# Performance work log

Measured on AMD Instinct MI355X. Metric: run time of the kernel, lower is better.

Reference implementation:

```python
import jax, jax.numpy as jnp
import numpy as np
from math import sqrt

N = 8192      # points
I = 16        # in_channels
H = 64        # hidden_units
O = 64        # out_channels
CUTS = 8      # conv MLP intermediate width
RADIUS = 9.0
GROUPS = 4    # GroupNorm groups
BLK = 128     # i-block size for tiled pairwise reduction (KeOps-style)


def _leaky(x):
    return jnp.where(x >= 0, x, 0.2 * x)


def _group_norm(f, w, b, eps=1e-5):
    # torch GroupNorm applied to (1, C, N): stats per group over (C//G channels x N points)
    n, c = f.shape
    g = f.reshape(n, GROUPS, c // GROUPS)
    m = g.mean(axis=(0, 2), keepdims=True)
    v = ((g - m) ** 2).mean(axis=(0, 2), keepdims=True)
    g = (g - m) * jax.lax.rsqrt(v + eps)
    return g.reshape(n, c) * w + b


def setup_inputs() -> dict:
    key = jax.random.key(0)
    ks = jax.random.split(key, 20)
    U = lambda k, s, lim: jax.random.uniform(k, s, minval=-lim, maxval=lim)
    points = jax.random.normal(ks[0], (N, 3), dtype=jnp.float32)
    nuv = jax.random.normal(ks[1], (N, 3, 3), dtype=jnp.float32)
    features = jax.random.normal(ks[2], (N, I), dtype=jnp.float32)
    # net_in (torch Linear default init)
    W_in1 = U(ks[3], (H, I), 1 / np.sqrt(I)); b_in1 = U(ks[4], (H,), 1 / np.sqrt(I))
    W_in2 = U(ks[5], (H, H), 1 / np.sqrt(H)); b_in2 = U(ks[6], (H,), 1 / np.sqrt(H))
    # conv MLP with custom init from the module
    A1 = jax.random.normal(ks[7], (CUTS, 3), dtype=jnp.float32)
    B1 = jax.random.uniform(ks[8], (CUTS,)) * 0.8 * jnp.sqrt((A1 ** 2).sum(-1))
    A2 = U(ks[9], (H, CUTS), 1 / np.sqrt(CUTS))
    B2 = jax.random.normal(ks[10], (H,)) * 0.5 * jnp.sqrt((A2 ** 2).sum(-1))
    # net_out
    W_out1 = U(ks[11], (O, H), 1 / np.sqrt(H)); b_out1 = U(ks[12], (O,), 1 / np.sqrt(H))
    W_out2 = U(ks[13], (O, O), 1 / np.sqrt(O)); b_out2 = U(ks[14], (O,), 1 / np.sqrt(O))
    return {
        "points": points, "nuv": nuv, "features": features,
        "W_in1": W_in1, "b_in1": b_in1, "W_in2": W_in2, "b_in2": b_in2,
        "gn_in_w": jnp.ones((H,), jnp.float32), "gn_in_b": jnp.zeros((H,), jnp.float32),
        "A1": A1, "B1": B1, "A2": A2, "B2": B2,
        "W_out1": W_out1, "b_out1": b_out1, "W_out2": W_out2, "b_out2": b_out2,
        "gn_out_w": jnp.ones((O,), jnp.float32), "gn_out_b": jnp.zeros((O,), jnp.float32),
    }


def _forward(points, nuv, features, W_in1, b_in1, W_in2, b_in2, gn_in_w, gn_in_b,
             A1, B1, A2, B2, W_out1, b_out1, W_out2, b_out2, gn_out_w, gn_out_b):
    # 1. net_in + GroupNorm
    f = _leaky(features @ W_in1.T + b_in1)
    f = _leaky(f @ W_in2.T + b_in2)
    f = _group_norm(f, gn_in_w, gn_in_b)          # (N, H)
    # 2. quasi-geodesic interaction, tiled over i-blocks (KeOps-style)
    pts = points / (sqrt(2.0) * RADIUS)
    normals = jax.lax.stop_gradient(nuv[:, 0, :])  # n_j is detached in the original
    nblk = N // BLK

    def body(carry, blk):
        xi, nuvi = blk                              # (B,3), (B,3,3)
        ni = nuvi[:, 0, :]                          # (B,3) n_i (not detached)
        diff = pts[None, :, :] - xi[:, None, :]     # (B,N,3) x_j - x_i
        dn = ni @ normals.T                         # (B,N) <n_i, n_j>
        d2 = (diff ** 2).sum(-1) * (2.0 - dn) ** 2  # pseudo-geodesic squared dist
        w = jnp.exp(-d2)                            # Gaussian window
        X = jnp.einsum('bij,bnj->bni', nuvi, diff)  # coords in local basis (B,N,3)
        h = jax.nn.relu(jnp.einsum('bnj,cj->bnc', X, A1) + B1)   # (B,N,CUTS)
        g = jax.nn.relu(jnp.einsum('bnc,hc->bnh', h, A2) + B2)   # (B,N,H)
        out = jnp.einsum('bn,bnh,nh->bh', w, g, f)  # sum_j w_ij * conv(P_ij) * f_j
        return carry, out

    _, outs = jax.lax.scan(
        body, None, (pts.reshape(nblk, BLK, 3), nuv.reshape(nblk, BLK, 3, 3)))
    f2 = outs.reshape(N, H)
    # 3. net_out + GroupNorm
    f2 = _leaky(f2 @ W_out1.T + b_out1)
    f2 = _leaky(f2 @ W_out2.T + b_out2)
    f2 = _group_norm(f2, gn_out_w, gn_out_b)       # (N, O)
    return f2


def reference(points, nuv, features, W_in1, b_in1, W_in2, b_in2, gn_in_w, gn_in_b,
              A1, B1, A2, B2, W_out1, b_out1, W_out2, b_out2, gn_out_w, gn_out_b):
    return _forward(points, nuv, features, W_in1, b_in1, W_in2, b_in2, gn_in_w, gn_in_b,
                    A1, B1, A2, B2, W_out1, b_out1, W_out2, b_out2, gn_out_w, gn_out_b)
```

## Files before the change

kernel.cpp:

```cpp
#include <hip/hip_runtime.h>
#include <hip/hip_bf16.h>
#include <stdint.h>


#define N_PTS   8192
#define CHUNK   64
#define NCHUNK  (N_PTS / CHUNK)
#define WPB     8
#define PSCALE  0.07856742013183861f
#define GN_CNT  (N_PTS * 16)

#define OFF_POINTS 0
#define OFF_NUV    24576
#define OFF_FEAT   98304
#define OFF_WIN1   229376
#define OFF_BIN1   230400
#define OFF_WIN2   230464
#define OFF_BIN2   234560
#define OFF_GNIW   234624
#define OFF_GNIB   234688
#define OFF_A1     234752
#define OFF_B1     234776
#define OFF_A2     234784
#define OFF_B2     235296
#define OFF_WOUT1  235360
#define OFF_BOUT1  239456
#define OFF_WOUT2  239520
#define OFF_BOUT2  243616
#define OFF_GNOW   243680
#define OFF_GNOB   243744
#define CVT_TOTAL  243808
#define NSEG 19

typedef _Float16 half2_t __attribute__((ext_vector_type(2)));
typedef _Float16 f16x8   __attribute__((ext_vector_type(8)));
typedef float    f32x2   __attribute__((ext_vector_type(2)));
typedef float    f32x4   __attribute__((ext_vector_type(4)));

struct InPtrs { const void* p[NSEG]; };

__device__ __forceinline__ float rfl(float x) {
  return __int_as_float(__builtin_amdgcn_readfirstlane(__float_as_int(x)));
}
__device__ __forceinline__ float leaky(float x) { return x > 0.f ? x : 0.2f * x; }

#if __has_builtin(__builtin_amdgcn_cvt_pkrtz)
__device__ __forceinline__ half2_t pk16(float a, float b) {
  return __builtin_bit_cast(half2_t, __builtin_amdgcn_cvt_pkrtz(a, b));
}
#else
__device__ __forceinline__ half2_t pk16(float a, float b) {
  half2_t r; r.x = (_Float16)a; r.y = (_Float16)b; return r;
}
#endif

__global__ __launch_bounds__(256) void prep_kernel(InPtrs ptrs, float* dst,
                                                   float* gstats) {
  if (blockIdx.x == 0 && threadIdx.x < 16) gstats[threadIdx.x] = 0.f;
  const uint32_t w0 = ((const uint32_t*)ptrs.p[7])[0];
  const bool bf = (w0 != 0x3F800000u);
  const int CUM[NSEG + 1] = {0, 24576, 98304, 229376, 230400, 230464, 234560,
                             234624, 234688, 234752, 234776, 234784, 235296,
                             235360, 239456, 239520, 243616, 243680, 243744,
                             243808};
  for (int e = blockIdx.x * 256 + threadIdx.x; e < CVT_TOTAL;
       e += gridDim.x * 256) {
    int s = 0;
#pragma unroll
    for (int i = 1; i < NSEG; ++i) s += (e >= CUM[i]) ? 1 : 0;
    const int rem = e - CUM[s];
    float v = bf ? __bfloat162float(((const __hip_bfloat16*)ptrs.p[s])[rem])
                 : ((const float*)ptrs.p[s])[rem];
    if (s == 0) v *= PSCALE;
    dst[e] = v;
  }
}

__global__ __launch_bounds__(256) void pack_kernel(
    const float* __restrict__ pool, float4* __restrict__ ppk,
    float4* __restrict__ npk) {
  const int n = blockIdx.x * 256 + threadIdx.x;
  const float px = pool[OFF_POINTS + n * 3 + 0];
  const float py = pool[OFF_POINTS + n * 3 + 1];
  const float pz = pool[OFF_POINTS + n * 3 + 2];
  float4 p; p.x = px; p.y = py; p.z = pz;
  p.w = fmaf(px, px, fmaf(py, py, pz * pz));
  ppk[n] = p;
  float4 q;
  q.x = pool[OFF_NUV + n * 9 + 0];
  q.y = pool[OFF_NUV + n * 9 + 1];
  q.z = pool[OFF_NUV + n * 9 + 2];
  q.w = 0.f;
  npk[n] = q;
}

__global__ __launch_bounds__(256) void mlp_in_kernel(
    const float* __restrict__ pool, float* __restrict__ fbuf) {
  __shared__ float ls[4][64];
  const int t = threadIdx.x, nl = t >> 6, h = t & 63;
  const int n = blockIdx.x * 4 + nl;
  const float4* fr = (const float4*)(pool + OFF_FEAT + n * 16);
  const float4* w1 = (const float4*)(pool + OFF_WIN1 + h * 16);
  float a = pool[OFF_BIN1 + h];
#pragma unroll
  for (int k = 0; k < 4; ++k) {
    const float4 x = fr[k], w = w1[k];
    a = fmaf(x.x, w.x, a); a = fmaf(x.y, w.y, a);
    a = fmaf(x.z, w.z, a); a = fmaf(x.w, w.w, a);
  }
  ls[nl][h] = leaky(a);
  __syncthreads();
  const float4* w2 = (const float4*)(pool + OFF_WIN2 + h * 64);
  const float4* lr = (const float4*)&ls[nl][0];
  float c = pool[OFF_BIN2 + h];
#pragma unroll
  for (int k = 0; k < 16; ++k) {
    const float4 x = lr[k], w = w2[k];
    c = fmaf(x.x, w.x, c); c = fmaf(x.y, w.y, c);
    c = fmaf(x.z, w.z, c); c = fmaf(x.w, w.w, c);
  }
  fbuf[n * 64 + h] = leaky(c);
}

__global__ __launch_bounds__(256) void mlp_out_kernel(
    const float* __restrict__ cbuf, const float* __restrict__ pool,
    float* __restrict__ obuf) {
  __shared__ float ls[4][64];
  const int t = threadIdx.x, nl = t >> 6, h = t & 63;
  const int n = blockIdx.x * 4 + nl;
  const float4* cr = (const float4*)(cbuf + n * 64);
  const float4* w1 = (const float4*)(pool + OFF_WOUT1 + h * 64);
  float a = pool[OFF_BOUT1 + h];
#pragma unroll
  for (int k = 0; k < 16; ++k) {
    const float4 x = cr[k], w = w1[k];
    a = fmaf(x.x, w.x, a); a = fmaf(x.y, w.y, a);
    a = fmaf(x.z, w.z, a); a = fmaf(x.w, w.w, a);
  }
  ls[nl][h] = leaky(a);
  __syncthreads();
  const float4* w2 = (const float4*)(pool + OFF_WOUT2 + h * 64);
  const float4* lr = (const float4*)&ls[nl][0];
  float c = pool[OFF_BOUT2 + h];
#pragma unroll
  for (int k = 0; k < 16; ++k) {
    const float4 x = lr[k], w = w2[k];
    c = fmaf(x.x, w.x, c); c = fmaf(x.y, w.y, c);
    c = fmaf(x.z, w.z, c); c = fmaf(x.w, w.w, c);
  }
  obuf[n * 64 + h] = leaky(c);
}

__global__ __launch_bounds__(256) void gn_stats_kernel(
    const float* __restrict__ buf, float* __restrict__ gstats) {
  __shared__ float red[8];
  const int t = threadIdx.x;
  const int g = (t & 63) >> 4;
  if (t < 8) red[t] = 0.f;
  float s = 0.f, q = 0.f;
  for (int idx = blockIdx.x * 256 + t; idx < N_PTS * 64; idx += 64 * 256) {
    const float v = buf[idx];
    s += v; q = fmaf(v, v, q);
  }
  __syncthreads();
  atomicAdd(&red[g], s);
  atomicAdd(&red[4 + g], q);
  __syncthreads();
  if (t < 8) atomicAdd(&gstats[t], red[t]);
}

__global__ __launch_bounds__(256) void gn_apply_Q_kernel(
    const float* __restrict__ buf, const float* __restrict__ gstats,
    const float* __restrict__ pool, float4* __restrict__ bufq) {
  __shared__ float tile[64][68];
  const int t = threadIdx.x;
  const int c = blockIdx.x;
  const int n0 = c * 64;
  const int rr = t >> 4;
  const int cc4 = (t & 15) * 4;
  const int g = cc4 >> 4;
  const float m = gstats[g] * (1.f / GN_CNT);
  const float v = gstats[4 + g] * (1.f / GN_CNT) - m * m;
  const float rs = rsqrtf(fmaxf(v, 0.f) + 1e-5f);
  const float4 gw = *(const float4*)&pool[OFF_GNIW + cc4];
  const float4 gb = *(const float4*)&pool[OFF_GNIB + cc4];
#pragma unroll
  for (int r = 0; r < 4; ++r) {
    const int row = rr + 16 * r;
    const float4 x = *(const float4*)&buf[(n0 + row) * 64 + cc4];
    float4 o;
    o.x = fmaf((x.x - m) * rs, gw.x, gb.x);
    o.y = fmaf((x.y - m) * rs, gw.y, gb.y);
    o.z = fmaf((x.z - m) * rs, gw.z, gb.z);
    o.w = fmaf((x.w - m) * rs, gw.w, gb.w);
    *(float4*)&tile[row][cc4] = o;
  }
  __syncthreads();
#pragma unroll
  for (int si = 0; si < 4; ++si) {
    const int s = t + 256 * si;
    const int region = s >> 6, lane = s & 63;
    const int jt = region >> 2, ht = region & 3;
    const int kg = lane >> 4, l15 = lane & 15;
    const int jb = 16 * jt + 4 * kg, h = 16 * ht + l15;
    float4 o;
    o.x = tile[jb + 0][h];
    o.y = tile[jb + 1][h];
    o.z = tile[jb + 2][h];
    o.w = tile[jb + 3][h];
    bufq[c * 1024 + s] = o;
  }
}

__global__ __launch_bounds__(256) void gn_apply_out_kernel(
    const float* __restrict__ buf, const float* __restrict__ gstats,
    const float* __restrict__ pool, void* __restrict__ out,
    const uint32_t* __restrict__ dref) {
  const bool bf = (dref[0] != 0x3F800000u);
  const int idx = blockIdx.x * 256 + threadIdx.x;
  const int h = idx & 63, g = h >> 4;
  const float m = gstats[g] * (1.f / GN_CNT);
  const float v = gstats[4 + g] * (1.f / GN_CNT) - m * m;
  const float rs = rsqrtf(fmaxf(v, 0.f) + 1e-5f);
  const float r = fmaf((buf[idx] - m) * rs, pool[OFF_GNOW + h], pool[OFF_GNOB + h]);
  if (bf) ((__hip_bfloat16*)out)[idx] = __float2bfloat16(r);
  else    ((float*)out)[idx] = r;
}

__global__ __launch_bounds__(512, 8) void conv_kernel(
    const float* __restrict__ pool, const float4* __restrict__ fq,
    float* __restrict__ cbuf, const float4* __restrict__ ppk,
    const float4* __restrict__ npk) {
  __shared__ float4 f_q[1024];

  const int t = threadIdx.x;
  const int lane = t & 63;
  const int b = blockIdx.x * WPB + (t >> 6);
  const int kg  = lane >> 4;
  const int l15 = lane & 15;
  const bool iskg0 = (kg == 0), iskg1 = (kg == 1);

  const float pbx = rfl(pool[OFF_POINTS + b * 3 + 0]);
  const float pby = rfl(pool[OFF_POINTS + b * 3 + 1]);
  const float pbz = rfl(pool[OFF_POINTS + b * 3 + 2]);
  float nb[9];
#pragma unroll
  for (int i = 0; i < 9; ++i) nb[i] = rfl(pool[OFF_NUV + b * 9 + i]);
  const float pbsq = rfl(fmaf(pbx, pbx, fmaf(pby, pby, pbz * pbz)));

  float mM[24], mc[8];
#pragma unroll
  for (int cc = 0; cc < 8; ++cc) {
    const float a0 = pool[OFF_A1 + cc * 3 + 0];
    const float a1 = pool[OFF_A1 + cc * 3 + 1];
    const float a2 = pool[OFF_A1 + cc * 3 + 2];
#pragma unroll
    for (int j = 0; j < 3; ++j)
      mM[cc * 3 + j] =
          rfl(fmaf(a0, nb[j], fmaf(a1, nb[3 + j], a2 * nb[6 + j])));
    mc[cc] = rfl(fmaf(-mM[cc * 3 + 0], pbx,
                 fmaf(-mM[cc * 3 + 1], pby,
                 fmaf(-mM[cc * 3 + 2], pbz, pool[OFF_B1 + cc]))));
  }

  f16x8 bfrag[4];
#pragma unroll
  for (int ht = 0; ht < 4; ++ht) {
    const int h = 16 * ht + l15;
#pragma unroll
    for (int i = 0; i < 8; ++i) {
      float v = 0.f;
      if (kg == 0) v = pool[OFF_A2 + h * 8 + i];
      else if (kg == 1 && i == 0) v = pool[OFF_B2 + h];
      bfrag[ht][i] = (_Float16)v;
    }
  }

  const f32x4 kzero = {0.f, 0.f, 0.f, 0.f};
  f32x2 acc01[4], acc23[4];
#pragma unroll
  for (int ht = 0; ht < 4; ++ht) {
    acc01[ht].x = 0.f; acc01[ht].y = 0.f;
    acc23[ht].x = 0.f; acc23[ht].y = 0.f;
  }

  for (int c = 0; c < NCHUNK; ++c) {
    const float4 fv0 = fq[c * 1024 + t];
    const float4 fv1 = fq[c * 1024 + t + 512];
    const float4 pv = ppk[c * CHUNK + lane];
    const float4 nv = npk[c * CHUNK + lane];

    __syncthreads();
    f_q[t]       = fv0;
    f_q[t + 512] = fv1;

    const float dotp = fmaf(pv.x, pbx, fmaf(pv.y, pby, pv.z * pbz));
    const float dd   = fmaf(-2.f, dotp, pv.w + pbsq);
    const float dn   = fmaf(nb[0], nv.x, fmaf(nb[1], nv.y, nb[2] * nv.z));
    const float ttv  = 2.f - dn;
    const float wexp = __expf(-dd * ttv * ttv);
    float hc[8];
#pragma unroll
    for (int cc = 0; cc < 8; ++cc)
      hc[cc] = wexp * fmaxf(fmaf(mM[cc * 3 + 0], pv.x,
                            fmaf(mM[cc * 3 + 1], pv.y,
                            fmaf(mM[cc * 3 + 2], pv.z, mc[cc]))), 0.f);
    float4 lo;
    lo.x = __builtin_bit_cast(float, pk16(hc[0], hc[1]));
    lo.y = __builtin_bit_cast(float, pk16(hc[2], hc[3]));
    lo.z = __builtin_bit_cast(float, pk16(hc[4], hc[5]));
    lo.w = __builtin_bit_cast(float, pk16(hc[6], hc[7]));
    const int pkw = __builtin_bit_cast(int, pk16(wexp, 0.f));

    __syncthreads();

#pragma unroll
    for (int jt = 0; jt < 4; ++jt) {
      const int src4 = ((jt << 4) | l15) << 2;
      const int b0 = __builtin_amdgcn_ds_bpermute(
          src4, __builtin_bit_cast(int, lo.x));
      const int b1 = __builtin_amdgcn_ds_bpermute(
          src4, __builtin_bit_cast(int, lo.y));
      const int b2 = __builtin_amdgcn_ds_bpermute(
          src4, __builtin_bit_cast(int, lo.z));
      const int b3 = __builtin_amdgcn_ds_bpermute(
          src4, __builtin_bit_cast(int, lo.w));
      const int bw = __builtin_amdgcn_ds_bpermute(src4, pkw);
      int4 afi;
      afi.x = iskg0 ? b0 : (iskg1 ? bw : 0);
      afi.y = iskg0 ? b1 : 0;
      afi.z = iskg0 ? b2 : 0;
      afi.w = iskg0 ? b3 : 0;
      const f16x8 af = __builtin_bit_cast(f16x8, afi);
#pragma unroll
      for (int ht = 0; ht < 4; ++ht) {
        const f32x4 D = __builtin_amdgcn_mfma_f32_16x16x32_f16(
            af, bfrag[ht], kzero, 0, 0, 0);
        const float4 fv = f_q[(jt * 4 + ht) * 64 + lane];
        f32x2 fq01, fq23, q01, q23;
        fq01.x = fv.x; fq01.y = fv.y;
        fq23.x = fv.z; fq23.y = fv.w;
        q01.x = fmaxf(D[0], 0.f); q01.y = fmaxf(D[1], 0.f);
        q23.x = fmaxf(D[2], 0.f); q23.y = fmaxf(D[3], 0.f);
        asm("v_pk_fma_f32 %0, %1, %2, %0"
            : "+v"(acc01[ht]) : "v"(fq01), "v"(q01));
        asm("v_pk_fma_f32 %0, %1, %2, %0"
            : "+v"(acc23[ht]) : "v"(fq23), "v"(q23));
      }
    }
  }

  float accf[4];
#pragma unroll
  for (int ht = 0; ht < 4; ++ht) {
    float a = (acc01[ht].x + acc01[ht].y) + (acc23[ht].x + acc23[ht].y);
    a += __shfl_xor(a, 16, 64);
    a += __shfl_xor(a, 32, 64);
    accf[ht] = a;
  }
  if (lane < 16) {
#pragma unroll
    for (int ht = 0; ht < 4; ++ht)
      cbuf[b * 64 + 16 * ht + lane] = accf[ht];
  }
}

extern "C" void kernel_launch(void* const* d_in, const int* in_sizes, int n_in,
                              void* d_out, int out_size, void* d_ws, size_t ws_size,
                              hipStream_t stream) {
  (void)in_sizes; (void)n_in; (void)out_size; (void)ws_size;
  const uint32_t* dref = (const uint32_t*)d_in[7];

  float* pool   = (float*)d_ws;
  float* fbuf   = pool + CVT_TOTAL;
  float* cbuf   = fbuf + N_PTS * 64;
  float* gstats = cbuf + N_PTS * 64;
  float* fbufq  = gstats + 16;
  float* ppk    = fbufq + N_PTS * 64;
  float* npk    = ppk + N_PTS * 4;

  InPtrs ptrs;
  for (int i = 0; i < NSEG; ++i) ptrs.p[i] = d_in[i];

  prep_kernel<<<256, 256, 0, stream>>>(ptrs, pool, gstats);
  pack_kernel<<<N_PTS / 256, 256, 0, stream>>>(pool, (float4*)ppk, (float4*)npk);
  mlp_in_kernel<<<N_PTS / 4, 256, 0, stream>>>(pool, fbuf);
  gn_stats_kernel<<<64, 256, 0, stream>>>(fbuf, gstats);
  gn_apply_Q_kernel<<<NCHUNK, 256, 0, stream>>>(fbuf, gstats, pool,
                                                (float4*)fbufq);
  conv_kernel<<<N_PTS / WPB, 512, 0, stream>>>(pool, (const float4*)fbufq,
                                               cbuf, (const float4*)ppk,
                                               (const float4*)npk);
  mlp_out_kernel<<<N_PTS / 4, 256, 0, stream>>>(cbuf, pool, fbuf);
  gn_stats_kernel<<<64, 256, 0, stream>>>(fbuf, gstats + 8);
  gn_apply_out_kernel<<<N_PTS * 64 / 256, 256, 0, stream>>>(
      fbuf, gstats + 8, pool, d_out, dref);
}
```

Baseline: 799.6 us.

## Stream feature chunks straight into LDS and simplify conv accumulation

The conv kernel now fills the per-chunk feature tile in shared memory with direct global-to-LDS loads instead of loading into registers and storing to LDS. The packed two-wide FMA accumulators written in inline asm are replaced by four scalar FMA chains, one accumulator per hidden tile, and the launch-bounds occupancy hint is relaxed. The aim is to cut register pressure and the VGPR round trip on feature staging. In exchange the loads may not be waited on before the ds_read, and the scalar FMA chains are serially dependent.

```diff
diff --git a/kernel.cpp b/kernel.cpp
--- a/kernel.cpp
+++ b/kernel.cpp
@@ -34,8 +34,10 @@
 
 typedef _Float16 half2_t __attribute__((ext_vector_type(2)));
 typedef _Float16 f16x8   __attribute__((ext_vector_type(8)));
-typedef float    f32x2   __attribute__((ext_vector_type(2)));
 typedef float    f32x4   __attribute__((ext_vector_type(4)));
+
+typedef const __attribute__((address_space(1))) uint32_t gu32_t;
+typedef __attribute__((address_space(3))) uint32_t lu32_t;
 
 struct InPtrs { const void* p[NSEG]; };
 
@@ -227,7 +229,7 @@
   else    ((float*)out)[idx] = r;
 }
 
-__global__ __launch_bounds__(512, 8) void conv_kernel(
+__global__ __launch_bounds__(512) void conv_kernel(
     const float* __restrict__ pool, const float4* __restrict__ fq,
     float* __restrict__ cbuf, const float4* __restrict__ ppk,
     const float4* __restrict__ npk) {
@@ -235,7 +237,8 @@
 
   const int t = threadIdx.x;
   const int lane = t & 63;
-  const int b = blockIdx.x * WPB + (t >> 6);
+  const int wv = t >> 6;
+  const int b = blockIdx.x * WPB + wv;
   const int kg  = lane >> 4;
   const int l15 = lane & 15;
   const bool iskg0 = (kg == 0), iskg1 = (kg == 1);
@@ -277,22 +280,20 @@
   }
 
   const f32x4 kzero = {0.f, 0.f, 0.f, 0.f};
-  f32x2 acc01[4], acc23[4];
-#pragma unroll
-  for (int ht = 0; ht < 4; ++ht) {
-    acc01[ht].x = 0.f; acc01[ht].y = 0.f;
-    acc23[ht].x = 0.f; acc23[ht].y = 0.f;
-  }
+  float acc[4] = {0.f, 0.f, 0.f, 0.f};
 
   for (int c = 0; c < NCHUNK; ++c) {
-    const float4 fv0 = fq[c * 1024 + t];
-    const float4 fv1 = fq[c * 1024 + t + 512];
     const float4 pv = ppk[c * CHUNK + lane];
     const float4 nv = npk[c * CHUNK + lane];
 
     __syncthreads();
-    f_q[t]       = fv0;
-    f_q[t + 512] = fv1;
+
+    __builtin_amdgcn_global_load_lds(
+        (gu32_t*)(fq + c * 1024 + t),
+        (lu32_t*)(&f_q[wv * 64]), 16, 0, 0);
+    __builtin_amdgcn_global_load_lds(
+        (gu32_t*)(fq + c * 1024 + 512 + t),
+        (lu32_t*)(&f_q[512 + wv * 64]), 16, 0, 0);
 
     const float dotp = fmaf(pv.x, pbx, fmaf(pv.y, pby, pv.z * pbz));
     const float dd   = fmaf(-2.f, dotp, pv.w + pbsq);
@@ -337,31 +338,23 @@
         const f32x4 D = __builtin_amdgcn_mfma_f32_16x16x32_f16(
             af, bfrag[ht], kzero, 0, 0, 0);
         const float4 fv = f_q[(jt * 4 + ht) * 64 + lane];
-        f32x2 fq01, fq23, q01, q23;
-        fq01.x = fv.x; fq01.y = fv.y;
-        fq23.x = fv.z; fq23.y = fv.w;
-        q01.x = fmaxf(D[0], 0.f); q01.y = fmaxf(D[1], 0.f);
-        q23.x = fmaxf(D[2], 0.f); q23.y = fmaxf(D[3], 0.f);
-        asm("v_pk_fma_f32 %0, %1, %2, %0"
-            : "+v"(acc01[ht]) : "v"(fq01), "v"(q01));
-        asm("v_pk_fma_f32 %0, %1, %2, %0"
-            : "+v"(acc23[ht]) : "v"(fq23), "v"(q23));
+        acc[ht] = fmaf(fv.x, fmaxf(D[0], 0.f), acc[ht]);
+        acc[ht] = fmaf(fv.y, fmaxf(D[1], 0.f), acc[ht]);
+        acc[ht] = fmaf(fv.z, fmaxf(D[2], 0.f), acc[ht]);
+        acc[ht] = fmaf(fv.w, fmaxf(D[3], 0.f), acc[ht]);
       }
     }
   }
 
-  float accf[4];
 #pragma unroll
   for (int ht = 0; ht < 4; ++ht) {
-    float a = (acc01[ht].x + acc01[ht].y) + (acc23[ht].x + acc23[ht].y);
-    a += __shfl_xor(a, 16, 64);
-    a += __shfl_xor(a, 32, 64);
-    accf[ht] = a;
+    acc[ht] += __shfl_xor(acc[ht], 16, 64);
+    acc[ht] += __shfl_xor(acc[ht], 32, 64);
   }
   if (lane < 16) {
 #pragma unroll
     for (int ht = 0; ht < 4; ++ht)
-      cbuf[b * 64 + 16 * ht + lane] = accf[ht];
+      cbuf[b * 64 + 16 * ht + lane] = acc[ht];
   }
 }
 
```

After: 1.055 ms. 32.0% more time.
